# Optimization experiments

Measured on AMD Instinct MI355X. Metric: run time of the kernel, lower is better.

Reference implementation:

```python
import jax, jax.numpy as jnp
import numpy as np

B, D = 65536, 1024

def setup_inputs() -> dict:
    key = jax.random.key(0)
    x = jax.random.normal(key, (B, D), dtype=jnp.float32)
    return {"x": x}

def reference(x) -> jnp.ndarray:
    d = x.shape[1]
    # suffix_norm[:, i] = ||x[:, i:]|| via reverse cumulative sum of squares (single O(D) pass)
    suffix_norm = jnp.sqrt(jnp.cumsum((x * x)[:, ::-1], axis=1)[:, ::-1])
    r = suffix_norm[:, :1]                                   # [B, 1] full norm
    phi = jnp.arccos(x[:, : d - 1] / suffix_norm[:, : d - 1])  # [B, D-1]
    # last angle gets sign correction from the final coordinate
    phi_last = jnp.where(x[:, -1] < 0, 2.0 * jnp.pi - phi[:, -1], phi[:, -1])
    return jnp.concatenate([r, phi[:, : d - 2], phi_last[:, None]], axis=1)
```

## Files before the change

kernel.cpp:

```cpp
#include <hip/hip_runtime.h>
#include <math.h>


#define D_DIM 1024
#define TPB 256

__global__ __launch_bounds__(TPB) void tohypersphere_kernel(
    const float* __restrict__ x, float* __restrict__ out) {
    const int t = threadIdx.x;
    const int lane = t & 63;
    const int wave = t >> 6;
    const size_t row_off = (size_t)blockIdx.x * D_DIM;

    const float4 v = ((const float4*)(x + row_off))[t];

    float s3 = v.w * v.w;
    float s2 = fmaf(v.z, v.z, s3);
    float s1 = fmaf(v.y, v.y, s2);
    float s0 = fmaf(v.x, v.x, s1);

    float tot = s0;
#pragma unroll
    for (int off = 1; off < 64; off <<= 1) {
        float n = __shfl_down(tot, off, 64);
        if (lane + off < 64) tot += n;
    }

    __shared__ float wave_tot[4];
    __shared__ float edge_xw[4];
    if (lane == 0) wave_tot[wave] = tot;
    if (lane == 63) edge_xw[wave] = v.w;
    __syncthreads();

    float after = 0.0f;
#pragma unroll
    for (int w = 0; w < 4; ++w)
        if (w > wave) after += wave_tot[w];

    const float incl = tot + after;
    const float excl = incl - s0;

    float xw_prev = __shfl_up(v.w, 1, 64);
    if (lane == 0 && wave > 0) xw_prev = edge_xw[wave - 1];

    const float suf0 = incl;
    const float suf1 = s1 + excl;
    const float suf2 = s2 + excl;

    auto ang = [](float num, float den) {
        float r = num * rsqrtf(den);
        r = fminf(1.0f, fmaxf(-1.0f, r));
        return acosf(r);
    };

    float o0, o1, o2, o3;
    o1 = ang(v.x, suf0);
    o2 = ang(v.y, suf1);
    o3 = ang(v.z, suf2);
    if (t == 0) {
        o0 = sqrtf(incl);
    } else {
        o0 = ang(xw_prev, fmaf(xw_prev, xw_prev, incl));
    }
    if (t == TPB - 1) {
        if (v.w < 0.0f) o3 = 6.283185307179586476f - o3;
    }

    ((float4*)(out + row_off))[t] = make_float4(o0, o1, o2, o3);
}

extern "C" void kernel_launch(void* const* d_in, const int* in_sizes, int n_in,
                              void* d_out, int out_size, void* d_ws, size_t ws_size,
                              hipStream_t stream) {
    const float* x = (const float*)d_in[0];
    float* out = (float*)d_out;
    const int B = in_sizes[0] / D_DIM;
    tohypersphere_kernel<<<B, TPB, 0, stream>>>(x, out);
}
```

Baseline: 409.6 us.

## Map one row per wavefront with 16 elements per lane and nontemporal stores

```diff
diff --git a/kernel.cpp b/kernel.cpp
--- a/kernel.cpp
+++ b/kernel.cpp
@@ -4,69 +4,77 @@
 
 #define D_DIM 1024
 #define TPB 256
+#define RPB 4
+#define EPT 16
+
+typedef float v4f __attribute__((ext_vector_type(4)));
+
+__device__ __forceinline__ float ang(float num, float den) {
+    float r = num * rsqrtf(den);
+    r = fminf(1.0f, fmaxf(-1.0f, r));
+    return acosf(r);
+}
 
 __global__ __launch_bounds__(TPB) void tohypersphere_kernel(
-    const float* __restrict__ x, float* __restrict__ out) {
-    const int t = threadIdx.x;
-    const int lane = t & 63;
-    const int wave = t >> 6;
-    const size_t row_off = (size_t)blockIdx.x * D_DIM;
+    const float* __restrict__ x, float* __restrict__ out, int n_rows) {
+    const int lane = threadIdx.x & 63;
+    const int wv   = threadIdx.x >> 6;
+    const int row  = blockIdx.x * RPB + wv;
+    if (row >= n_rows) return;
 
-    const float4 v = ((const float4*)(x + row_off))[t];
+    const size_t off = (size_t)row * D_DIM + (size_t)lane * EPT;
 
-    float s3 = v.w * v.w;
-    float s2 = fmaf(v.z, v.z, s3);
-    float s1 = fmaf(v.y, v.y, s2);
-    float s0 = fmaf(v.x, v.x, s1);
+    const float4* __restrict__ xp = (const float4*)(x + off);
+    const float4 va = xp[0];
+    const float4 vb = xp[1];
+    const float4 vc = xp[2];
+    const float4 vd = xp[3];
 
-    float tot = s0;
+    float e[EPT];
+    e[0]  = va.x; e[1]  = va.y; e[2]  = va.z; e[3]  = va.w;
+    e[4]  = vb.x; e[5]  = vb.y; e[6]  = vb.z; e[7]  = vb.w;
+    e[8]  = vc.x; e[9]  = vc.y; e[10] = vc.z; e[11] = vc.w;
+    e[12] = vd.x; e[13] = vd.y; e[14] = vd.z; e[15] = vd.w;
+
+    float ls[EPT];
+    ls[EPT - 1] = e[EPT - 1] * e[EPT - 1];
 #pragma unroll
-    for (int off = 1; off < 64; off <<= 1) {
-        float n = __shfl_down(tot, off, 64);
-        if (lane + off < 64) tot += n;
+    for (int k = EPT - 2; k >= 0; --k) ls[k] = fmaf(e[k], e[k], ls[k + 1]);
+
+    float tot = ls[0];
+#pragma unroll
+    for (int o = 1; o < 64; o <<= 1) {
+        float n = __shfl_down(tot, o, 64);
+        if (lane + o < 64) tot += n;
+    }
+    const float incl = tot;
+    const float excl = incl - ls[0];
+
+    const float xprev = __shfl_up(e[EPT - 1], 1, 64);
+
+    float og[EPT];
+    if (lane == 0) {
+        og[0] = sqrtf(incl);
+    } else {
+        og[0] = ang(xprev, fmaf(xprev, xprev, incl));
+    }
+#pragma unroll
+    for (int m = 1; m < EPT; ++m) {
+        og[m] = ang(e[m - 1], ls[m - 1] + excl);
+    }
+    if (lane == 63 && e[EPT - 1] < 0.0f) {
+        og[EPT - 1] = 6.283185307179586476f - og[EPT - 1];
     }
 
-    __shared__ float wave_tot[4];
-    __shared__ float edge_xw[4];
-    if (lane == 0) wave_tot[wave] = tot;
-    if (lane == 63) edge_xw[wave] = v.w;
-    __syncthreads();
-
-    float after = 0.0f;
-#pragma unroll
-    for (int w = 0; w < 4; ++w)
-        if (w > wave) after += wave_tot[w];
-
-    const float incl = tot + after;
-    const float excl = incl - s0;
-
-    float xw_prev = __shfl_up(v.w, 1, 64);
-    if (lane == 0 && wave > 0) xw_prev = edge_xw[wave - 1];
-
-    const float suf0 = incl;
-    const float suf1 = s1 + excl;
-    const float suf2 = s2 + excl;
-
-    auto ang = [](float num, float den) {
-        float r = num * rsqrtf(den);
-        r = fminf(1.0f, fmaxf(-1.0f, r));
-        return acosf(r);
-    };
-
-    float o0, o1, o2, o3;
-    o1 = ang(v.x, suf0);
-    o2 = ang(v.y, suf1);
-    o3 = ang(v.z, suf2);
-    if (t == 0) {
-        o0 = sqrtf(incl);
-    } else {
-        o0 = ang(xw_prev, fmaf(xw_prev, xw_prev, incl));
-    }
-    if (t == TPB - 1) {
-        if (v.w < 0.0f) o3 = 6.283185307179586476f - o3;
-    }
-
-    ((float4*)(out + row_off))[t] = make_float4(o0, o1, o2, o3);
+    v4f* __restrict__ op = (v4f*)(out + off);
+    v4f t0 = {og[0],  og[1],  og[2],  og[3]};
+    v4f t1 = {og[4],  og[5],  og[6],  og[7]};
+    v4f t2 = {og[8],  og[9],  og[10], og[11]};
+    v4f t3 = {og[12], og[13], og[14], og[15]};
+    __builtin_nontemporal_store(t0, op + 0);
+    __builtin_nontemporal_store(t1, op + 1);
+    __builtin_nontemporal_store(t2, op + 2);
+    __builtin_nontemporal_store(t3, op + 3);
 }
 
 extern "C" void kernel_launch(void* const* d_in, const int* in_sizes, int n_in,
@@ -75,5 +83,6 @@
     const float* x = (const float*)d_in[0];
     float* out = (float*)d_out;
     const int B = in_sizes[0] / D_DIM;
-    tohypersphere_kernel<<<B, TPB, 0, stream>>>(x, out);
+    const int grid = (B + RPB - 1) / RPB;
+    tohypersphere_kernel<<<grid, TPB, 0, stream>>>(x, out, B);
 }
```

New measurement: 541.5 us. +32.2%, slower.
